# Kernel tuning notes

Hardware: AMD Instinct MI355X
Metric: run time of the kernel (lower is better)

## Reference

```python
import jax, jax.numpy as jnp
import numpy as np

DIM = 768
HID = 1536
EPS = 1e-12
SCALE = float(np.sqrt(DIM))


def _layernorm(x, gamma, beta):
    mu = jnp.mean(x, axis=-1, keepdims=True)
    var = jnp.mean(jnp.square(x - mu), axis=-1, keepdims=True)
    return (x - mu) * jax.lax.rsqrt(var + EPS) * gamma + beta


def setup_inputs() -> dict:
    key = jax.random.key(0)
    ks = jax.random.split(key, 16)
    s = 1.0 / np.sqrt(DIM)
    sh = 1.0 / np.sqrt(HID)
    x = jax.random.normal(ks[0], (8, 2048, DIM), dtype=jnp.float32)
    return {
        "x": x,
        "Wq": jax.random.uniform(ks[1], (DIM, DIM), jnp.float32, -s, s),
        "bq": jax.random.uniform(ks[2], (DIM,), jnp.float32, -s, s),
        "Wk": jax.random.uniform(ks[3], (DIM, DIM), jnp.float32, -s, s),
        "bk": jax.random.uniform(ks[4], (DIM,), jnp.float32, -s, s),
        "Wv": jax.random.uniform(ks[5], (DIM, DIM), jnp.float32, -s, s),
        "bv": jax.random.uniform(ks[6], (DIM,), jnp.float32, -s, s),
        "Wp": jax.random.uniform(ks[7], (DIM, DIM), jnp.float32, -s, s),
        "bp": jax.random.uniform(ks[8], (DIM,), jnp.float32, -s, s),
        "g1": jnp.ones((DIM,), jnp.float32),
        "be1": jnp.zeros((DIM,), jnp.float32),
        "W1": jax.random.uniform(ks[9], (HID, DIM), jnp.float32, -s, s),
        "b1": jax.random.uniform(ks[10], (HID,), jnp.float32, -s, s),
        "W2": jax.random.uniform(ks[11], (DIM, HID), jnp.float32, -sh, sh),
        "b2": jax.random.uniform(ks[12], (DIM,), jnp.float32, -sh, sh),
        "g2": jnp.ones((DIM,), jnp.float32),
        "be2": jnp.zeros((DIM,), jnp.float32),
    }


def reference(x, Wq, bq, Wk, bk, Wv, bv, Wp, bp, g1, be1, W1, b1, W2, b2, g2, be2):
    # NOTE: original code does NOT split into heads; single full-dim bmm attention.
    Q = jnp.einsum("bsd,ed->bse", x, Wq) + bq  # [B,S,D]
    K = jnp.einsum("bsd,ed->bse", x, Wk) + bk
    V = jnp.einsum("bsd,ed->bse", x, Wv) + bv
    alpha = jnp.einsum("bqd,bkd->bqk", Q, K) / SCALE  # [B,S,S]
    alpha = jax.nn.softmax(alpha, axis=-1)
    attn = jnp.einsum("bqk,bkd->bqd", alpha, V)
    attn = jnp.einsum("bsd,ed->bse", attn, Wp) + bp  # linear_proj
    h = _layernorm(x + attn, g1, be1)
    mlp = jax.nn.gelu(jnp.einsum("bsd,hd->bsh", h, W1) + b1, approximate=False)
    mlp = jnp.einsum("bsh,dh->bsd", mlp, W2) + b2
    return _layernorm(h + mlp, g2, be2)
```

## Files before the change

kernel.cpp:

```cpp
#include <hip/hip_runtime.h>
#include <math.h>

#define D_MODEL 768
#define D_HID   1536
#define N_BATCH 8
#define SEQLEN  2048
#define NROWS   (N_BATCH*SEQLEN)

typedef unsigned short u16;
typedef unsigned char  u8;
typedef __attribute__((ext_vector_type(8))) short bfrag;
typedef __attribute__((ext_vector_type(4))) float facc;

__device__ __forceinline__ u16 f2bf(float f) {
  unsigned u = __float_as_uint(f);
  u += 0x7fffu + ((u >> 16) & 1u);
  return (u16)(u >> 16);
}
__device__ __forceinline__ float bf2f(u16 u) {
  return __uint_as_float((unsigned)u << 16);
}
__device__ __forceinline__ u8 f2fp8(float f) {
  return (u8)(__builtin_amdgcn_cvt_pk_fp8_f32(f, f, 0, 0) & 0xff);
}

__device__ __forceinline__ void async16(const void* g, void* l) {
  __builtin_amdgcn_global_load_lds((const __attribute__((address_space(1))) void*)g,
                                   (__attribute__((address_space(3))) void*)l,
                                   16, 0, 0);
}
__device__ __forceinline__ void wg_barrier() {
  asm volatile("" ::: "memory");
  __builtin_amdgcn_s_barrier();
  asm volatile("" ::: "memory");
}
#define VMCNT(n) asm volatile("s_waitcnt vmcnt(" #n ")" ::: "memory")

__global__ __launch_bounds__(256) void cvt_all(
    const float* __restrict__ x,  const float* __restrict__ Wq,
    const float* __restrict__ Wk, const float* __restrict__ Wv,
    const float* __restrict__ Wp, const float* __restrict__ W1,
    const float* __restrict__ W2, const float* __restrict__ bq,
    const float* __restrict__ bk, const float* __restrict__ bv,
    u16* __restrict__ XB, u16* __restrict__ WQKV, u16* __restrict__ WPB,
    u16* __restrict__ W1B, u16* __restrict__ W2B, float* __restrict__ BQKV,
    float* __restrict__ LSUM) {
  long i = (long)blockIdx.x * 256 + threadIdx.x;
  const float* src; u16* dst; long off;
  if      (i < 3145728) { src = x;  dst = XB;             off = i; }
  else if (i < 3293184) { src = Wq; dst = WQKV;           off = i - 3145728; }
  else if (i < 3440640) { src = Wk; dst = WQKV + 589824;  off = i - 3293184; }
  else if (i < 3588096) { src = Wv; dst = WQKV + 1179648; off = i - 3440640; }
  else if (i < 3735552) { src = Wp; dst = WPB;            off = i - 3588096; }
  else if (i < 4030464) { src = W1; dst = W1B;            off = i - 3735552; }
  else if (i < 4325376) { src = W2; dst = W2B;            off = i - 4030464; }
  else if (i < 4325952) {
    long j = i - 4325376;
    const float* s = (j < 192) ? bq : (j < 384) ? bk : bv;
    long o = (j < 192) ? j : (j < 384) ? j - 192 : j - 384;
    ((float4*)BQKV)[j] = ((const float4*)s)[o];
    return;
  } else if (i < 4330048) {
    float4 zz = {0.f, 0.f, 0.f, 0.f};
    ((float4*)LSUM)[i - 4325952] = zz;
    return;
  } else return;
  float4 v = ((const float4*)src)[off];
  ushort4 o4;
  o4.x = f2bf(v.x); o4.y = f2bf(v.y); o4.z = f2bf(v.z); o4.w = f2bf(v.w);
  *reinterpret_cast<ushort4*>(dst + off * 4) = o4;
}

enum { EPI_EXP = 1, EPI_DIV = 2, EPI_GELU = 4, EPI_QKV = 5, EPI_RES = 6 };

template<int EPI>
__global__ __launch_bounds__(256, 3)
void gemm_bt(const u16* __restrict__ Aall, const u16* __restrict__ Ball,
             void* __restrict__ Cout,
             int M, int N, int K,
             long sA, long sB, long sC,
             const float* __restrict__ bias,
             const u16* __restrict__ resid,
             float* __restrict__ lsum,
             float scale)
{
  __shared__ __align__(16) char smem[49152];
  const int z = blockIdx.z;
  const u16* A = Aall + (long)z * sA;
  const u16* B = Ball + (long)z * sB;
  const int bm = blockIdx.x, bn = blockIdx.y;
  const int tid = (int)threadIdx.x;
  const int lane = tid & 63, wv = tid >> 6;
  const int wr = wv >> 1, wc = wv & 1;

  facc acc[4][4] = {};

  const int srow2 = tid >> 2;
  const int c4 = tid & 3;
  const int skey = (srow2 >> 1) & 3;
  const int sc = ((c4 ^ skey) << 3);
  const u16* Abase = A + (long)(bm * 128) * K;
  const u16* Bbase = B + (long)(bn * 128) * K;
  const int fr = lane & 15, g0 = lane >> 4;
  const int rkey = (fr >> 1) & 3;
  const int nt = K >> 5;

  auto STAGE = [&](int t, int b) {
    char* Asb = smem + b * 16384;
    char* Bsb = Asb + 8192;
    const long k0 = (long)t << 5;
#pragma unroll
    for (int p = 0; p < 2; ++p) {
      async16(Abase + (long)(p * 64 + srow2) * K + k0 + sc, Asb + p * 4096 + tid * 16);
      async16(Bbase + (long)(p * 64 + srow2) * K + k0 + sc, Bsb + p * 4096 + tid * 16);
    }
  };

  STAGE(0, 0); STAGE(1, 1);
  int rb_ = 0, sb_ = 2;
  for (int t = 0; t < nt; ++t) {
    if (t < nt - 1) { VMCNT(4); } else { VMCNT(0); }
    wg_barrier();
    if (t + 2 < nt) STAGE(t + 2, sb_);
    const u16* As = (const u16*)(smem + rb_ * 16384);
    const u16* Bs = As + 4096;
    bfrag af[4], bf[4];
#pragma unroll
    for (int i = 0; i < 4; ++i) {
      const int r = wr * 64 + i * 16 + fr;
      af[i] = *(const bfrag*)(As + r * 32 + ((g0 ^ rkey) << 3));
    }
#pragma unroll
    for (int j = 0; j < 4; ++j) {
      const int r = wc * 64 + j * 16 + fr;
      bf[j] = *(const bfrag*)(Bs + r * 32 + ((g0 ^ rkey) << 3));
    }
    __builtin_amdgcn_s_setprio(1);
#pragma unroll
    for (int i = 0; i < 4; ++i)
#pragma unroll
      for (int j = 0; j < 4; ++j)
        acc[i][j] = __builtin_amdgcn_mfma_f32_16x16x32_bf16(af[i], bf[j], acc[i][j], 0, 0, 0);
    __builtin_amdgcn_s_setprio(0);
    rb_ = (rb_ == 2) ? 0 : rb_ + 1;
    sb_ = (sb_ == 2) ? 0 : sb_ + 1;
  }
  wg_barrier();

  const int rb = bm * 128 + wr * 64;
  const int cb = bn * 128 + wc * 64;
  const int quad = lane >> 4;

  if constexpr (EPI == EPI_QKV) {
    const int c64 = bn * 2 + wc;
    const int which = c64 / 12;
    float bj[4];
#pragma unroll
    for (int j = 0; j < 4; ++j) bj[j] = bias[cb + j * 16 + fr];
    if (which == 2) {
      u8* VT_ = (u8*)resid;
      const int zb = rb >> 11;
      const int seqb = (rb & 2047) + quad * 4;
      const int dimb = (c64 - 24) * 64;
#pragma unroll
      for (int i = 0; i < 4; ++i) {
#pragma unroll
        for (int j = 0; j < 4; ++j) {
          const int dim = dimb + j * 16 + fr;
          unsigned v01 = __builtin_amdgcn_cvt_pk_fp8_f32(acc[i][j][0] + bj[j],
                                                         acc[i][j][1] + bj[j], 0, 0);
          unsigned v23 = __builtin_amdgcn_cvt_pk_fp8_f32(acc[i][j][2] + bj[j],
                                                         acc[i][j][3] + bj[j], 0, 0);
          unsigned w = (v01 & 0xffffu) | (v23 << 16);
          *reinterpret_cast<unsigned*>(VT_ + (long)zb * D_MODEL * SEQLEN +
                                       (long)dim * SEQLEN + seqb + i * 16) = w;
        }
      }
      return;
    }
    u8* ep8 = (u8*)(smem + wv * 8192);
    u8* Cg = (u8*)Cout + (long)which * NROWS * D_MODEL;
    const int cbo = (c64 - which * 12) * 64;
#pragma unroll
    for (int i = 0; i < 4; ++i)
#pragma unroll
      for (int r = 0; r < 4; ++r) {
        const int lrow = i * 16 + quad * 4 + r;
#pragma unroll
        for (int j = 0; j < 4; ++j)
          ep8[lrow * 64 + j * 16 + fr] = f2fp8(acc[i][j][r] + bj[j]);
      }
#pragma unroll
    for (int it = 0; it < 4; ++it) {
      const int lr = it * 16 + (lane >> 2);
      const int ch = (lane & 3) << 4;
      int4 d = *(const int4*)(ep8 + lr * 64 + ch);
      *reinterpret_cast<int4*>(Cg + (long)(rb + lr) * D_MODEL + cbo + ch) = d;
    }
  } else if constexpr (EPI == EPI_GELU) {
    u16* ep16 = (u16*)(smem + wv * 8192);
    u16* Cg = (u16*)Cout + (long)z * sC;
    float bj[4];
#pragma unroll
    for (int j = 0; j < 4; ++j) bj[j] = bias[cb + j * 16 + fr];
#pragma unroll
    for (int i = 0; i < 4; ++i) {
#pragma unroll
      for (int r = 0; r < 4; ++r) {
        const int lrow = i * 16 + quad * 4 + r;
#pragma unroll
        for (int j = 0; j < 4; ++j) {
          float t = acc[i][j][r] + bj[j];
          float y = 0.7978845608f * (t + 0.044715f * t * t * t);
          float e = __expf(-2.f * fabsf(y));
          float th = (1.f - e) / (1.f + e);
          th = (y < 0.f) ? -th : th;
          ep16[lrow * 64 + j * 16 + fr] = f2bf(0.5f * t * (1.f + th));
        }
      }
    }
#pragma unroll
    for (int it = 0; it < 8; ++it) {
      const int lr = it * 8 + (lane >> 3);
      const int ch = (lane & 7) << 3;
      int4 d = *(const int4*)(ep16 + lr * 64 + ch);
      *reinterpret_cast<int4*>(Cg + (long)(rb + lr) * N + cb + ch) = d;
    }
  } else {
    float* ep32 = (float*)(smem + wv * 8192);
    u16* Cg = (u16*)Cout;
#pragma unroll
    for (int h = 0; h < 2; ++h) {
#pragma unroll
      for (int i2 = 0; i2 < 2; ++i2) {
        const int i = h * 2 + i2;
#pragma unroll
        for (int r = 0; r < 4; ++r) {
          const int lrow = i2 * 16 + quad * 4 + r;
#pragma unroll
          for (int j = 0; j < 4; ++j)
            ep32[lrow * 64 + j * 16 + fr] = acc[i][j][r];
        }
      }
#pragma unroll
      for (int it = 0; it < 8; ++it) {
        const int lr = it * 4 + (lane >> 4);
        const int ch = (lane & 15) << 2;
        float4 d = *(const float4*)(ep32 + lr * 64 + ch);
        const int row = rb + h * 32 + lr;
        const int gcol = cb + ch;
        const long gi = (long)row * N + gcol;
        ushort4 rv = *(const ushort4*)(resid + gi);
        float4 bb = *(const float4*)(bias + gcol);
        ushort4 o;
        o.x = f2bf(d.x + bb.x + bf2f(rv.x));
        o.y = f2bf(d.y + bb.y + bf2f(rv.y));
        o.z = f2bf(d.z + bb.z + bf2f(rv.z));
        o.w = f2bf(d.w + bb.w + bf2f(rv.w));
        *reinterpret_cast<ushort4*>(Cg + gi) = o;
      }
      wg_barrier();
    }
  }
  (void)lsum; (void)scale; (void)M;
}

template<int EPI>
__global__ __launch_bounds__(256, 3)
void gemm_f8(const u8* __restrict__ Aall, const u8* __restrict__ Ball,
             void* __restrict__ Cout,
             int M, int N, int K,
             long sA, long sB, long sC,
             float* __restrict__ lsum, float scale)
{
  __shared__ __align__(16) char smem[49152];
  const int z = blockIdx.z;
  const u8* A = Aall + (long)z * sA;
  const u8* B = Ball + (long)z * sB;
  const int bm = blockIdx.x, bn = blockIdx.y;
  const int tid = (int)threadIdx.x;
  const int lane = tid & 63, wv = tid >> 6;
  const int wr = wv >> 1, wc = wv & 1;

  facc acc[4][4] = {};

  const int srow2 = tid >> 2;
  const int c4 = tid & 3;
  const int skey = (srow2 >> 1) & 3;
  const int scb = ((c4 ^ skey) << 4);
  const u8* Abase = A + (long)(bm * 128) * K;
  const u8* Bbase = B + (long)(bn * 128) * K;
  const int fr = lane & 15, g0 = lane >> 4;
  const int rkey = (fr >> 1) & 3;
  const int nt = K >> 6;

  auto STAGE = [&](int t, int b) {
    char* Asb = smem + b * 16384;
    char* Bsb = Asb + 8192;
    const long k0 = (long)t << 6;
#pragma unroll
    for (int p = 0; p < 2; ++p) {
      async16(Abase + (long)(p * 64 + srow2) * K + k0 + scb, Asb + p * 4096 + tid * 16);
      async16(Bbase + (long)(p * 64 + srow2) * K + k0 + scb, Bsb + p * 4096 + tid * 16);
    }
  };

  STAGE(0, 0); STAGE(1, 1);
  int rb_ = 0, sb_ = 2;
  for (int t = 0; t < nt; ++t) {
    if (t < nt - 1) { VMCNT(4); } else { VMCNT(0); }
    wg_barrier();
    if (t + 2 < nt) STAGE(t + 2, sb_);
    const u8* As = (const u8*)(smem + rb_ * 16384);
    const u8* Bs = As + 8192;
#pragma unroll
    for (int s = 0; s < 2; ++s) {
      long af[4], bf[4];
      const int cc = (s * 2 + (g0 >> 1)) ^ rkey;
      const int h8 = (g0 & 1) << 3;
#pragma unroll
      for (int i = 0; i < 4; ++i) {
        const int r = wr * 64 + i * 16 + fr;
        af[i] = *(const long*)(As + r * 64 + (cc << 4) + h8);
      }
#pragma unroll
      for (int j = 0; j < 4; ++j) {
        const int r = wc * 64 + j * 16 + fr;
        bf[j] = *(const long*)(Bs + r * 64 + (cc << 4) + h8);
      }
      __builtin_amdgcn_s_setprio(1);
#pragma unroll
      for (int i = 0; i < 4; ++i)
#pragma unroll
        for (int j = 0; j < 4; ++j)
          acc[i][j] = __builtin_amdgcn_mfma_f32_16x16x32_fp8_fp8(af[i], bf[j], acc[i][j], 0, 0, 0);
      __builtin_amdgcn_s_setprio(0);
    }
    rb_ = (rb_ == 2) ? 0 : rb_ + 1;
    sb_ = (sb_ == 2) ? 0 : sb_ + 1;
  }
  wg_barrier();

  const int rb = bm * 128 + wr * 64;
  const int cb = bn * 128 + wc * 64;
  const int quad = lane >> 4;

  if constexpr (EPI == EPI_EXP) {
    u8* ep8 = (u8*)(smem + wv * 4096);
    u8* Cg = (u8*)Cout + (long)z * sC;
#pragma unroll
    for (int i = 0; i < 4; ++i) {
#pragma unroll
      for (int r = 0; r < 4; ++r) {
        const int lrow = i * 16 + quad * 4 + r;
        const int row = rb + lrow;
        float rs = 0.f;
#pragma unroll
        for (int j = 0; j < 4; ++j) {
          float e = __expf(acc[i][j][r] * scale - 3.0f);
          rs += e;
          ep8[lrow * 64 + j * 16 + fr] = f2fp8(e);
        }
        rs += __shfl_xor(rs, 1);
        rs += __shfl_xor(rs, 2);
        rs += __shfl_xor(rs, 4);
        rs += __shfl_xor(rs, 8);
        if (fr == 0) atomicAdd(&lsum[(long)z * M + row], rs);
      }
    }
#pragma unroll
    for (int it = 0; it < 4; ++it) {
      const int lr = it * 16 + (lane >> 2);
      const int ch = (lane & 3) << 4;
      int4 d = *(const int4*)(ep8 + lr * 64 + ch);
      *reinterpret_cast<int4*>(Cg + (long)(rb + lr) * N + cb + ch) = d;
    }
  } else {
    u16* ep16 = (u16*)(smem + wv * 4096);
    u16* Cg = (u16*)Cout + (long)z * sC;
#pragma unroll
    for (int h = 0; h < 2; ++h) {
#pragma unroll
      for (int i2 = 0; i2 < 2; ++i2) {
        const int i = h * 2 + i2;
#pragma unroll
        for (int r = 0; r < 4; ++r) {
          const int lrow = i2 * 16 + quad * 4 + r;
          const int row = rb + h * 32 + lrow;
          const float inv = 1.f / lsum[(long)z * M + row];
#pragma unroll
          for (int j = 0; j < 4; ++j)
            ep16[lrow * 64 + j * 16 + fr] = f2bf(acc[i][j][r] * inv);
        }
      }
#pragma unroll
      for (int it = 0; it < 4; ++it) {
        const int lr = it * 8 + (lane >> 3);
        const int ch = (lane & 7) << 3;
        int4 d = *(const int4*)(ep16 + lr * 64 + ch);
        *reinterpret_cast<int4*>(Cg + (long)(rb + h * 32 + lr) * N + cb + ch) = d;
      }
      wg_barrier();
    }
  }
}

__global__ __launch_bounds__(192) void layernorm_rows(const u16* __restrict__ in,
                                                      const float* __restrict__ gamma,
                                                      const float* __restrict__ beta,
                                                      float* __restrict__ outf,
                                                      u16* __restrict__ outb) {
  const int row = blockIdx.x;
  const int t = threadIdx.x;
  ushort4 uv = ((const ushort4*)(in + (long)row * D_MODEL))[t];
  float v0 = bf2f(uv.x), v1 = bf2f(uv.y), v2 = bf2f(uv.z), v3 = bf2f(uv.w);
  float s1 = v0 + v1 + v2 + v3;
  float s2 = v0 * v0 + v1 * v1 + v2 * v2 + v3 * v3;
#pragma unroll
  for (int o = 32; o; o >>= 1) { s1 += __shfl_xor(s1, o); s2 += __shfl_xor(s2, o); }
  __shared__ float r1[3], r2[3];
  const int wv = t >> 6, ln = t & 63;
  if (ln == 0) { r1[wv] = s1; r2[wv] = s2; }
  __syncthreads();
  s1 = r1[0] + r1[1] + r1[2];
  s2 = r2[0] + r2[1] + r2[2];
  const float mu = s1 * (1.f / 768.f);
  const float var = s2 * (1.f / 768.f) - mu * mu;
  const float rstd = rsqrtf(var + 1e-12f);
  float4 gv = ((const float4*)gamma)[t];
  float4 bv = ((const float4*)beta)[t];
  float o0 = (v0 - mu) * rstd * gv.x + bv.x;
  float o1 = (v1 - mu) * rstd * gv.y + bv.y;
  float o2 = (v2 - mu) * rstd * gv.z + bv.z;
  float o3 = (v3 - mu) * rstd * gv.w + bv.w;
  if (outf) {
    float4 ov = {o0, o1, o2, o3};
    ((float4*)(outf + (long)row * D_MODEL))[t] = ov;
  }
  if (outb) {
    ushort4 ob;
    ob.x = f2bf(o0); ob.y = f2bf(o1); ob.z = f2bf(o2); ob.w = f2bf(o3);
    ((ushort4*)(outb + (long)row * D_MODEL))[t] = ob;
  }
}

static const size_t OFF_WP   = 0;
static const size_t OFF_W1   = 1179648;
static const size_t OFF_W2   = 3538944;
static const size_t OFF_LSUM = 5898240;
static const size_t OFF_BQKV = 5963776;
static const size_t OFF_QB   = 6291456;
static const size_t OFF_KB   = 18874368;
static const size_t OFF_VT   = 31457280;
static const size_t OFF_EB   = 44040192;
static const size_t OFF_CTX  = 77594624;
static const size_t OFF_XB   = 102760448;
static const size_t OFF_WQKV = 127926272;
static const size_t OFF_M1B  = 131465216;

extern "C" void kernel_launch(void* const* d_in, const int* in_sizes, int n_in,
                              void* d_out, int out_size, void* d_ws, size_t ws_size,
                              hipStream_t stream) {
  const float* x   = (const float*)d_in[0];
  const float* Wq  = (const float*)d_in[1];
  const float* bq  = (const float*)d_in[2];
  const float* Wk  = (const float*)d_in[3];
  const float* bk  = (const float*)d_in[4];
  const float* Wv  = (const float*)d_in[5];
  const float* bv  = (const float*)d_in[6];
  const float* Wp  = (const float*)d_in[7];
  const float* bp  = (const float*)d_in[8];
  const float* g1  = (const float*)d_in[9];
  const float* be1 = (const float*)d_in[10];
  const float* W1  = (const float*)d_in[11];
  const float* b1  = (const float*)d_in[12];
  const float* W2  = (const float*)d_in[13];
  const float* b2  = (const float*)d_in[14];
  const float* g2  = (const float*)d_in[15];
  const float* be2 = (const float*)d_in[16];

  char* ws = (char*)d_ws;
  u16*   WPB  = (u16*)(ws + OFF_WP);
  u16*   W1B  = (u16*)(ws + OFF_W1);
  u16*   W2B  = (u16*)(ws + OFF_W2);
  float* LSUM = (float*)(ws + OFF_LSUM);
  float* BQKV = (float*)(ws + OFF_BQKV);
  u8*    QB   = (u8*)(ws + OFF_QB);
  u8*    KB   = (u8*)(ws + OFF_KB);
  u8*    VT   = (u8*)(ws + OFF_VT);
  u8*    EB   = (u8*)(ws + OFF_EB);
  u16*   CTX  = (u16*)(ws + OFF_CTX);
  u16*   XB   = (u16*)(ws + OFF_XB);
  u16*   WQKV = (u16*)(ws + OFF_WQKV);
  u16*   M1B  = (u16*)(ws + OFF_M1B);
  u16*   PB   = (u16*)(ws + OFF_QB);
  u16*   HB   = (u16*)(ws + OFF_EB);
  u16*   M2B  = (u16*)(ws + OFF_CTX);

  dim3 blk(256), blkl(192);

  cvt_all<<<dim3(16915), blk, 0, stream>>>(x, Wq, Wk, Wv, Wp, W1, W2, bq, bk, bv,
                                           XB, WQKV, WPB, W1B, W2B, BQKV, LSUM);

  gemm_bt<EPI_QKV><<<dim3(128, 18, 1), blk, 0, stream>>>(XB, WQKV, QB,
      NROWS, 3 * D_MODEL, D_MODEL, 0, 0, 0, BQKV, (const u16*)VT, nullptr, 0.f);

  const float sc = 1.0f / sqrtf((float)D_MODEL);
  gemm_f8<EPI_EXP><<<dim3(16, 16, 8), blk, 0, stream>>>(QB, KB, EB,
      SEQLEN, SEQLEN, D_MODEL,
      (long)SEQLEN * D_MODEL, (long)SEQLEN * D_MODEL, (long)SEQLEN * SEQLEN,
      LSUM, sc);
  gemm_f8<EPI_DIV><<<dim3(16, 6, 8), blk, 0, stream>>>(EB, VT, CTX,
      SEQLEN, D_MODEL, SEQLEN,
      (long)SEQLEN * SEQLEN, (long)D_MODEL * SEQLEN, (long)SEQLEN * D_MODEL,
      LSUM, 0.f);
  gemm_bt<EPI_RES><<<dim3(128, 6, 1), blk, 0, stream>>>(CTX, WPB, PB,
      NROWS, D_MODEL, D_MODEL, 0, 0, 0, bp, XB, nullptr, 0.f);
  layernorm_rows<<<dim3(NROWS), blkl, 0, stream>>>(PB, g1, be1, nullptr, HB);
  gemm_bt<EPI_GELU><<<dim3(128, 12, 1), blk, 0, stream>>>(HB, W1B, M1B,
      NROWS, D_HID, D_MODEL, 0, 0, 0, b1, nullptr, nullptr, 0.f);
  gemm_bt<EPI_RES><<<dim3(128, 6, 1), blk, 0, stream>>>(M1B, W2B, M2B,
      NROWS, D_MODEL, D_HID, 0, 0, 0, b2, HB, nullptr, 0.f);
  layernorm_rows<<<dim3(NROWS), blkl, 0, stream>>>(M2B, g2, be2, (float*)d_out, nullptr);

  (void)in_sizes; (void)n_in; (void)out_size; (void)ws_size;
}
```

Baseline: 466.7 us.

## Use 512-thread 128x256 tile for QKV GEMM; double-buffer score GEMM

```diff
diff --git a/kernel.cpp b/kernel.cpp
--- a/kernel.cpp
+++ b/kernel.cpp
@@ -73,6 +73,127 @@
 
 enum { EPI_EXP = 1, EPI_DIV = 2, EPI_GELU = 4, EPI_QKV = 5, EPI_RES = 6 };
 
+__global__ __launch_bounds__(512, 2)
+void gemm_bt512(const u16* __restrict__ Aall, const u16* __restrict__ Ball,
+                void* __restrict__ Cout,
+                int M, int N, int K,
+                long sA, long sB, long sC,
+                const float* __restrict__ bias,
+                const u16* __restrict__ residVT,
+                float* __restrict__ lsum, float scale)
+{
+  __shared__ __align__(16) char smem[73728];
+  const u16* A = Aall;
+  const u16* B = Ball;
+  const int bm = blockIdx.x, bn = blockIdx.y;
+  const int tid = (int)threadIdx.x;
+  const int lane = tid & 63, wv = tid >> 6;
+  const int wr = wv >> 2, wc = wv & 3;
+
+  facc acc[4][4] = {};
+
+  const int srow2 = tid >> 2;
+  const int c4 = tid & 3;
+  const int skey = (srow2 >> 1) & 3;
+  const int sc = ((c4 ^ skey) << 3);
+  const u16* Abase = A + (long)(bm * 128) * K;
+  const u16* Bbase = B + (long)(bn * 256) * K;
+  const int fr = lane & 15, g0 = lane >> 4;
+  const int rkey = (fr >> 1) & 3;
+  const int nt = K >> 5;
+
+  auto STAGE = [&](int t, int b) {
+    char* Asb = smem + b * 24576;
+    char* Bsb = Asb + 8192;
+    const long k0 = (long)t << 5;
+    async16(Abase + (long)srow2 * K + k0 + sc, Asb + tid * 16);
+#pragma unroll
+    for (int p = 0; p < 2; ++p)
+      async16(Bbase + (long)(p * 128 + srow2) * K + k0 + sc, Bsb + p * 8192 + tid * 16);
+  };
+
+  STAGE(0, 0); STAGE(1, 1);
+  int rb_ = 0, sb_ = 2;
+  for (int t = 0; t < nt; ++t) {
+    if (t < nt - 1) { VMCNT(3); } else { VMCNT(0); }
+    wg_barrier();
+    if (t + 2 < nt) STAGE(t + 2, sb_);
+    const u16* As = (const u16*)(smem + rb_ * 24576);
+    const u16* Bs = As + 4096;
+    bfrag af[4], bf[4];
+#pragma unroll
+    for (int i = 0; i < 4; ++i) {
+      const int r = wr * 64 + i * 16 + fr;
+      af[i] = *(const bfrag*)(As + r * 32 + ((g0 ^ rkey) << 3));
+    }
+#pragma unroll
+    for (int j = 0; j < 4; ++j) {
+      const int r = wc * 64 + j * 16 + fr;
+      bf[j] = *(const bfrag*)(Bs + r * 32 + ((g0 ^ rkey) << 3));
+    }
+    __builtin_amdgcn_s_setprio(1);
+#pragma unroll
+    for (int i = 0; i < 4; ++i)
+#pragma unroll
+      for (int j = 0; j < 4; ++j)
+        acc[i][j] = __builtin_amdgcn_mfma_f32_16x16x32_bf16(af[i], bf[j], acc[i][j], 0, 0, 0);
+    __builtin_amdgcn_s_setprio(0);
+    rb_ = (rb_ == 2) ? 0 : rb_ + 1;
+    sb_ = (sb_ == 2) ? 0 : sb_ + 1;
+  }
+  wg_barrier();
+
+  const int rb = bm * 128 + wr * 64;
+  const int cb = bn * 256 + wc * 64;
+  const int quad = lane >> 4;
+  const int c64 = bn * 4 + wc;
+  const int which = c64 / 12;
+  float bj[4];
+#pragma unroll
+  for (int j = 0; j < 4; ++j) bj[j] = bias[cb + j * 16 + fr];
+  if (which == 2) {
+    u8* VT_ = (u8*)residVT;
+    const int zb = rb >> 11;
+    const int seqb = (rb & 2047) + quad * 4;
+    const int dimb = (c64 - 24) * 64;
+#pragma unroll
+    for (int i = 0; i < 4; ++i) {
+#pragma unroll
+      for (int j = 0; j < 4; ++j) {
+        const int dim = dimb + j * 16 + fr;
+        unsigned v01 = __builtin_amdgcn_cvt_pk_fp8_f32(acc[i][j][0] + bj[j],
+                                                       acc[i][j][1] + bj[j], 0, 0);
+        unsigned v23 = __builtin_amdgcn_cvt_pk_fp8_f32(acc[i][j][2] + bj[j],
+                                                       acc[i][j][3] + bj[j], 0, 0);
+        unsigned w = (v01 & 0xffffu) | (v23 << 16);
+        *reinterpret_cast<unsigned*>(VT_ + (long)zb * D_MODEL * SEQLEN +
+                                     (long)dim * SEQLEN + seqb + i * 16) = w;
+      }
+    }
+    return;
+  }
+  u8* ep8 = (u8*)(smem + wv * 8192);
+  u8* Cg = (u8*)Cout + (long)which * NROWS * D_MODEL;
+  const int cbo = (c64 - which * 12) * 64;
+#pragma unroll
+  for (int i = 0; i < 4; ++i)
+#pragma unroll
+    for (int r = 0; r < 4; ++r) {
+      const int lrow = i * 16 + quad * 4 + r;
+#pragma unroll
+      for (int j = 0; j < 4; ++j)
+        ep8[lrow * 64 + j * 16 + fr] = f2fp8(acc[i][j][r] + bj[j]);
+    }
+#pragma unroll
+  for (int it = 0; it < 4; ++it) {
+    const int lr = it * 16 + (lane >> 2);
+    const int ch = (lane & 3) << 4;
+    int4 d = *(const int4*)(ep8 + lr * 64 + ch);
+    *reinterpret_cast<int4*>(Cg + (long)(rb + lr) * D_MODEL + cbo + ch) = d;
+  }
+  (void)lsum; (void)scale; (void)M; (void)sA; (void)sB; (void)sC;
+}
+
 template<int EPI>
 __global__ __launch_bounds__(256, 3)
 void gemm_bt(const u16* __restrict__ Aall, const u16* __restrict__ Ball,
@@ -151,53 +272,7 @@
   const int cb = bn * 128 + wc * 64;
   const int quad = lane >> 4;
 
-  if constexpr (EPI == EPI_QKV) {
-    const int c64 = bn * 2 + wc;
-    const int which = c64 / 12;
-    float bj[4];
-#pragma unroll
-    for (int j = 0; j < 4; ++j) bj[j] = bias[cb + j * 16 + fr];
-    if (which == 2) {
-      u8* VT_ = (u8*)resid;
-      const int zb = rb >> 11;
-      const int seqb = (rb & 2047) + quad * 4;
-      const int dimb = (c64 - 24) * 64;
-#pragma unroll
-      for (int i = 0; i < 4; ++i) {
-#pragma unroll
-        for (int j = 0; j < 4; ++j) {
-          const int dim = dimb + j * 16 + fr;
-          unsigned v01 = __builtin_amdgcn_cvt_pk_fp8_f32(acc[i][j][0] + bj[j],
-                                                         acc[i][j][1] + bj[j], 0, 0);
-          unsigned v23 = __builtin_amdgcn_cvt_pk_fp8_f32(acc[i][j][2] + bj[j],
-                                                         acc[i][j][3] + bj[j], 0, 0);
-          unsigned w = (v01 & 0xffffu) | (v23 << 16);
-          *reinterpret_cast<unsigned*>(VT_ + (long)zb * D_MODEL * SEQLEN +
-                                       (long)dim * SEQLEN + seqb + i * 16) = w;
-        }
-      }
-      return;
-    }
-    u8* ep8 = (u8*)(smem + wv * 8192);
-    u8* Cg = (u8*)Cout + (long)which * NROWS * D_MODEL;
-    const int cbo = (c64 - which * 12) * 64;
-#pragma unroll
-    for (int i = 0; i < 4; ++i)
-#pragma unroll
-      for (int r = 0; r < 4; ++r) {
-        const int lrow = i * 16 + quad * 4 + r;
-#pragma unroll
-        for (int j = 0; j < 4; ++j)
-          ep8[lrow * 64 + j * 16 + fr] = f2fp8(acc[i][j][r] + bj[j]);
-      }
-#pragma unroll
-    for (int it = 0; it < 4; ++it) {
-      const int lr = it * 16 + (lane >> 2);
-      const int ch = (lane & 3) << 4;
-      int4 d = *(const int4*)(ep8 + lr * 64 + ch);
-      *reinterpret_cast<int4*>(Cg + (long)(rb + lr) * D_MODEL + cbo + ch) = d;
-    }
-  } else if constexpr (EPI == EPI_GELU) {
+  if constexpr (EPI == EPI_GELU) {
     u16* ep16 = (u16*)(smem + wv * 8192);
     u16* Cg = (u16*)Cout + (long)z * sC;
     float bj[4];
@@ -262,18 +337,18 @@
       wg_barrier();
     }
   }
-  (void)lsum; (void)scale; (void)M;
-}
-
-template<int EPI>
-__global__ __launch_bounds__(256, 3)
+  (void)lsum; (void)scale; (void)M; (void)resid; (void)bias;
+}
+
+template<int EPI, int DEPTH>
+__global__ __launch_bounds__(256, 6 - DEPTH)
 void gemm_f8(const u8* __restrict__ Aall, const u8* __restrict__ Ball,
              void* __restrict__ Cout,
              int M, int N, int K,
              long sA, long sB, long sC,
              float* __restrict__ lsum, float scale)
 {
-  __shared__ __align__(16) char smem[49152];
+  __shared__ __align__(16) char smem[DEPTH * 16384];
   const int z = blockIdx.z;
   const u8* A = Aall + (long)z * sA;
   const u8* B = Ball + (long)z * sB;
@@ -305,13 +380,8 @@
     }
   };
 
-  STAGE(0, 0); STAGE(1, 1);
-  int rb_ = 0, sb_ = 2;
-  for (int t = 0; t < nt; ++t) {
-    if (t < nt - 1) { VMCNT(4); } else { VMCNT(0); }
-    wg_barrier();
-    if (t + 2 < nt) STAGE(t + 2, sb_);
-    const u8* As = (const u8*)(smem + rb_ * 16384);
+  auto COMPUTE = [&](int buf) {
+    const u8* As = (const u8*)(smem + buf * 16384);
     const u8* Bs = As + 8192;
 #pragma unroll
     for (int s = 0; s < 2; ++s) {
@@ -336,10 +406,30 @@
           acc[i][j] = __builtin_amdgcn_mfma_f32_16x16x32_fp8_fp8(af[i], bf[j], acc[i][j], 0, 0, 0);
       __builtin_amdgcn_s_setprio(0);
     }
-    rb_ = (rb_ == 2) ? 0 : rb_ + 1;
-    sb_ = (sb_ == 2) ? 0 : sb_ + 1;
-  }
-  wg_barrier();
+  };
+
+  if constexpr (DEPTH == 3) {
+    STAGE(0, 0); STAGE(1, 1);
+    int rb_ = 0, sb_ = 2;
+    for (int t = 0; t < nt; ++t) {
+      if (t < nt - 1) { VMCNT(4); } else { VMCNT(0); }
+      wg_barrier();
+      if (t + 2 < nt) STAGE(t + 2, sb_);
+      COMPUTE(rb_);
+      rb_ = (rb_ == 2) ? 0 : rb_ + 1;
+      sb_ = (sb_ == 2) ? 0 : sb_ + 1;
+    }
+    wg_barrier();
+  } else {
+    STAGE(0, 0); STAGE(1, 1);
+    for (int t = 0; t < nt; ++t) {
+      if (t < nt - 1) { VMCNT(4); } else { VMCNT(0); }
+      wg_barrier();
+      COMPUTE(t & 1);
+      wg_barrier();
+      if (t + 2 < nt) STAGE(t + 2, t & 1);
+    }
+  }
 
   const int rb = bm * 128 + wr * 64;
   const int cb = bn * 128 + wc * 64;
@@ -497,20 +587,20 @@
   u16*   HB   = (u16*)(ws + OFF_EB);
   u16*   M2B  = (u16*)(ws + OFF_CTX);
 
-  dim3 blk(256), blkl(192);
+  dim3 blk(256), blkg(512), blkl(192);
 
   cvt_all<<<dim3(16915), blk, 0, stream>>>(x, Wq, Wk, Wv, Wp, W1, W2, bq, bk, bv,
                                            XB, WQKV, WPB, W1B, W2B, BQKV, LSUM);
 
-  gemm_bt<EPI_QKV><<<dim3(128, 18, 1), blk, 0, stream>>>(XB, WQKV, QB,
+  gemm_bt512<<<dim3(128, 9, 1), blkg, 0, stream>>>(XB, WQKV, QB,
       NROWS, 3 * D_MODEL, D_MODEL, 0, 0, 0, BQKV, (const u16*)VT, nullptr, 0.f);
 
   const float sc = 1.0f / sqrtf((float)D_MODEL);
-  gemm_f8<EPI_EXP><<<dim3(16, 16, 8), blk, 0, stream>>>(QB, KB, EB,
+  gemm_f8<EPI_EXP, 2><<<dim3(16, 16, 8), blk, 0, stream>>>(QB, KB, EB,
       SEQLEN, SEQLEN, D_MODEL,
       (long)SEQLEN * D_MODEL, (long)SEQLEN * D_MODEL, (long)SEQLEN * SEQLEN,
       LSUM, sc);
-  gemm_f8<EPI_DIV><<<dim3(16, 6, 8), blk, 0, stream>>>(EB, VT, CTX,
+  gemm_f8<EPI_DIV, 3><<<dim3(16, 6, 8), blk, 0, stream>>>(EB, VT, CTX,
       SEQLEN, D_MODEL, SEQLEN,
       (long)SEQLEN * SEQLEN, (long)D_MODEL * SEQLEN, (long)SEQLEN * D_MODEL,
       LSUM, 0.f);
```

Result: no change. 464.4 us (-0.5%).
